# Optimization experiments

Measured on AMD Instinct MI355X. Metric: run time of the kernel, lower is better.

The kernel has to match this reference:

```python
import jax, jax.numpy as jnp
import numpy as np

N_NODES = 50000
N_EDGES = 800000
D_IN = 64
D_OUT = 64


def setup_inputs() -> dict:
    key = jax.random.key(0)
    k1, k2, k3, k4 = jax.random.split(key, 4)
    x = jax.random.normal(k1, (N_NODES, D_IN), dtype=jnp.float32)
    src = jax.random.randint(k2, (N_EDGES,), 0, N_NODES, dtype=jnp.int64)
    dst = jax.random.randint(k3, (N_EDGES,), 0, N_NODES, dtype=jnp.int64)
    W = jax.random.normal(k4, (D_IN, D_OUT), dtype=jnp.float32) / np.sqrt(D_IN)
    b = jnp.zeros((D_OUT,), dtype=jnp.float32)
    return {"x": x, "src": src, "dst": dst, "W": W, "b": b}


def reference(x, src, dst, W, b):
    # DGL GraphConv, norm='both': out = D_in^{-1/2} A D_out^{-1/2} x W + b
    n = x.shape[0]
    ones = jnp.ones(src.shape[0], dtype=x.dtype)
    out_deg = jax.ops.segment_sum(ones, src, num_segments=n)  # out-degree of each node
    in_deg = jax.ops.segment_sum(ones, dst, num_segments=n)   # in-degree of each node
    norm_src = jax.lax.rsqrt(jnp.clip(out_deg, 1.0))          # [N]
    norm_dst = jax.lax.rsqrt(jnp.clip(in_deg, 1.0))           # [N]
    h = x * norm_src[:, None]                                 # [N, D_in]
    msg = jnp.take(h, src, axis=0)                            # [E, D_in] gather
    agg = jax.ops.segment_sum(msg, dst, num_segments=n)       # [N, D_in] scatter-add
    agg = agg * norm_dst[:, None]
    return agg @ W + b                                        # [N, D_out]
```

## Files before the change

### kernel.cpp

```cpp
#include <hip/hip_runtime.h>
#include <hip/hip_fp16.h>

#define N_NODES 50000
#define N_EDGES 800000
#define D 64

#define SLICES 100
#define I4S    2000
#define NI4    200000
#define NWORDS 12512

typedef float vfloat2 __attribute__((ext_vector_type(2)));

#define CTR_OFF    0
#define BASE_OFF   256
#define END_OFF    200320
#define SNORM_OFF  400384
#define DNORM_OFF  600448
#define SSRC_OFF   800512
#define OCC_OFF    4000768
#define PART_OFF   4800768
#define YA_OFF     14810368
#define YB_OFF     18010624

__global__ __launch_bounds__(256) void degree_occ_kernel(const int4* __restrict__ src4,
                                                         const int4* __restrict__ dst4,
                                                         unsigned int* __restrict__ partial,
                                                         uchar4* __restrict__ occ4,
                                                         int* __restrict__ ctr) {
    __shared__ unsigned int hist[NWORDS];
    int tid = threadIdx.x;
    if (blockIdx.x == 0 && tid == 0) *ctr = 0;
    uint4* h4 = (uint4*)hist;
    for (int i = tid; i < NWORDS / 4; i += 256) h4[i] = make_uint4(0, 0, 0, 0);
    __syncthreads();

    int role  = blockIdx.x & 1;
    int slice = blockIdx.x >> 1;
    int beg = slice * I4S, end = beg + I4S;
    if (role == 0) {
        for (int i = beg + tid; i < end; i += 256) {
            int4 v = src4[i];
            atomicAdd(&hist[v.x >> 2], 1u << ((v.x & 3) * 8));
            atomicAdd(&hist[v.y >> 2], 1u << ((v.y & 3) * 8));
            atomicAdd(&hist[v.z >> 2], 1u << ((v.z & 3) * 8));
            atomicAdd(&hist[v.w >> 2], 1u << ((v.w & 3) * 8));
        }
    } else {
        for (int i = beg + tid; i < end; i += 256) {
            int4 v = dst4[i];
            unsigned int o0 = (atomicAdd(&hist[v.x >> 2], 1u << ((v.x & 3) * 8)) >> ((v.x & 3) * 8)) & 0xFFu;
            unsigned int o1 = (atomicAdd(&hist[v.y >> 2], 1u << ((v.y & 3) * 8)) >> ((v.y & 3) * 8)) & 0xFFu;
            unsigned int o2 = (atomicAdd(&hist[v.z >> 2], 1u << ((v.z & 3) * 8)) >> ((v.z & 3) * 8)) & 0xFFu;
            unsigned int o3 = (atomicAdd(&hist[v.w >> 2], 1u << ((v.w & 3) * 8)) >> ((v.w & 3) * 8)) & 0xFFu;
            occ4[i] = make_uchar4((unsigned char)o0, (unsigned char)o1,
                                  (unsigned char)o2, (unsigned char)o3);
        }
    }
    __syncthreads();

    uint4* p4 = (uint4*)(partial + (size_t)blockIdx.x * NWORDS);
    for (int i = tid; i < NWORDS / 4; i += 256) p4[i] = h4[i];
}

__global__ __launch_bounds__(256) void merge_scan_kernel(unsigned int* __restrict__ partial,
                                                         int* __restrict__ base,
                                                         int* __restrict__ rend,
                                                         float* __restrict__ snorm,
                                                         float* __restrict__ dnorm,
                                                         int* __restrict__ ctr) {
    int w = blockIdx.x * blockDim.x + threadIdx.x;
    int lane = threadIdx.x & 63;
    unsigned int accin = 0, accout = 0;
    if (w < 12500) {
        unsigned int* po = partial + w;
        unsigned int* pd = partial + NWORDS + w;
#pragma unroll 4
        for (int s = 0; s < SLICES; s++) {
            size_t off = (size_t)(2 * s) * NWORDS;
            accout += po[off];
            unsigned int v = pd[off];
            pd[off] = accin;
            accin += v;
        }
    }
    int d0 = accin & 0xFF, d1 = (accin >> 8) & 0xFF,
        d2 = (accin >> 16) & 0xFF, d3 = (accin >> 24) & 0xFF;
    int tsum = d0 + d1 + d2 + d3;
    int run = tsum;
#pragma unroll
    for (int off = 1; off < 64; off <<= 1) {
        int v = __shfl_up(run, off);
        if (lane >= off) run += v;
    }
    int wtot = __shfl(run, 63);
    int wbase = 0;
    if (lane == 63) wbase = atomicAdd(ctr, wtot);
    wbase = __shfl(wbase, 63);
    if (w < 12500) {
        int b0 = wbase + run - tsum;
        int b1 = b0 + d0, b2 = b1 + d1, b3 = b2 + d2;
        ((int4*)base)[w] = make_int4(b0, b1, b2, b3);
        ((int4*)rend)[w] = make_int4(b1, b2, b3, b3 + d3);
        ((float4*)dnorm)[w] = make_float4(rsqrtf(fmaxf((float)d0, 1.f)),
                                          rsqrtf(fmaxf((float)d1, 1.f)),
                                          rsqrtf(fmaxf((float)d2, 1.f)),
                                          rsqrtf(fmaxf((float)d3, 1.f)));
        int o0 = accout & 0xFF, o1 = (accout >> 8) & 0xFF,
            o2 = (accout >> 16) & 0xFF, o3 = (accout >> 24) & 0xFF;
        ((float4*)snorm)[w] = make_float4(rsqrtf(fmaxf((float)o0, 1.f)),
                                          rsqrtf(fmaxf((float)o1, 1.f)),
                                          rsqrtf(fmaxf((float)o2, 1.f)),
                                          rsqrtf(fmaxf((float)o3, 1.f)));
    }
}

#define FYBLK 1024
__global__ __launch_bounds__(256, 4) void filly_kernel(const int4* __restrict__ src4,
                                                       const int4* __restrict__ dst4,
                                                       const uchar4* __restrict__ occ4,
                                                       const unsigned int* __restrict__ partial,
                                                       const int* __restrict__ base,
                                                       int* __restrict__ ssrc,
                                                       const float* __restrict__ x,
                                                       const float* __restrict__ snorm,
                                                       const float* __restrict__ W,
                                                       __half* __restrict__ yA,
                                                       __half* __restrict__ yB) {
    int tid = blockIdx.x * blockDim.x + threadIdx.x;
    int lane = threadIdx.x & 63;

    if (tid < NI4) {
        int s = tid / I4S;
        const unsigned int* pref = partial + (size_t)(2 * s + 1) * NWORDS;
        int4 sv = src4[tid], tv = dst4[tid];
        uchar4 oc = occ4[tid];
#define FILL_ONE(T, S, O)                                                     \
        {                                                                     \
            int t = (T); int sh = (t & 3) * 8;                                \
            int p = base[t] + (int)((pref[t >> 2] >> sh) & 0xFFu) + (int)(O); \
            ssrc[p] = (S);                                                    \
        }
        FILL_ONE(tv.x, sv.x, oc.x)
        FILL_ONE(tv.y, sv.y, oc.y)
        FILL_ONE(tv.z, sv.z, oc.z)
        FILL_ONE(tv.w, sv.w, oc.w)
#undef FILL_ONE
    }

    float Wreg[D];
#pragma unroll
    for (int k = 0; k < D; k++) Wreg[k] = W[k * D + lane];
    __half* yh = (lane < 32) ? yA : yB;
    int jl = lane & 31;
    int wave = tid >> 6;
    const int nwaves = FYBLK * 4;
    for (int n = wave; n < N_NODES; n += nwaves) {
        float hv = x[(size_t)n * D + lane] * snorm[n];
        int hb = __float_as_int(hv);
        float p0 = 0.f, p1 = 0.f, p2 = 0.f, p3 = 0.f;
#pragma unroll
        for (int k = 0; k < D; k += 4) {
            p0 = fmaf(__int_as_float(__builtin_amdgcn_readlane(hb, k + 0)), Wreg[k + 0], p0);
            p1 = fmaf(__int_as_float(__builtin_amdgcn_readlane(hb, k + 1)), Wreg[k + 1], p1);
            p2 = fmaf(__int_as_float(__builtin_amdgcn_readlane(hb, k + 2)), Wreg[k + 2], p2);
            p3 = fmaf(__int_as_float(__builtin_amdgcn_readlane(hb, k + 3)), Wreg[k + 3], p3);
        }
        yh[(size_t)n * 32 + jl] = __float2half((p0 + p1) + (p2 + p3));
    }
}

#define GBLK 2048
__global__ __launch_bounds__(256, 8) void gather_kernel(const __half2* __restrict__ yA,
                                                        const __half2* __restrict__ yB,
                                                        const int* __restrict__ ssrc,
                                                        const int* __restrict__ base,
                                                        const int* __restrict__ rend,
                                                        const float* __restrict__ dnorm,
                                                        const float* __restrict__ bias,
                                                        float* __restrict__ out) {
    int lane = threadIdx.x & 63;
    int q = lane >> 4;
    int c = lane & 15;
    int pass = blockIdx.x & 1;
    int pblk = blockIdx.x >> 1;
    int wave = (pblk << 2) | (threadIdx.x >> 6);
    const int nwaves = (GBLK / 2) * 4;

    float2 b2 = ((const float2*)bias)[(pass << 4) + c];
    const __half2* ycol = (pass ? yB : yA) + c;

#define ACC(A, F) { (A).x += (F).x; (A).y += (F).y; }

    for (int n = wave; n < N_NODES; n += nwaves) {
        int beg = base[n], end = rend[n];
        float dn = dnorm[n];
        float2 a0 = make_float2(0.f, 0.f), a1 = a0, a2 = a0, a3 = a0;
        int i = beg;
        for (; i + 16 <= end; i += 16) {
            int s0 = ssrc[i + q],      s1 = ssrc[i + 4 + q];
            int s2 = ssrc[i + 8 + q],  s3 = ssrc[i + 12 + q];
            float2 f0 = __half22float2(ycol[(size_t)s0 * 16]);
            float2 f1 = __half22float2(ycol[(size_t)s1 * 16]);
            float2 f2 = __half22float2(ycol[(size_t)s2 * 16]);
            float2 f3 = __half22float2(ycol[(size_t)s3 * 16]);
            ACC(a0, f0) ACC(a1, f1) ACC(a2, f2) ACC(a3, f3)
        }
        for (; i + 4 <= end; i += 4) {
            int s = ssrc[i + q];
            float2 f = __half22float2(ycol[(size_t)s * 16]);
            ACC(a0, f)
        }
        int rem = end - i;
        if (q < rem) {
            int s = ssrc[i + q];
            float2 f = __half22float2(ycol[(size_t)s * 16]);
            ACC(a1, f)
        }
        float2 t;
        t.x = (a0.x + a1.x) + (a2.x + a3.x);
        t.y = (a0.y + a1.y) + (a2.y + a3.y);
        t.x += __shfl(t.x, lane ^ 16); t.y += __shfl(t.y, lane ^ 16);
        t.x += __shfl(t.x, lane ^ 32); t.y += __shfl(t.y, lane ^ 32);
        if (q == 0) {
            vfloat2 o;
            o.x = fmaf(t.x, dn, b2.x);
            o.y = fmaf(t.y, dn, b2.y);
            __builtin_nontemporal_store(o, (vfloat2*)(out + (size_t)n * D + (pass << 5)) + c);
        }
    }
#undef ACC
}

extern "C" void kernel_launch(void* const* d_in, const int* in_sizes, int n_in,
                              void* d_out, int out_size, void* d_ws, size_t ws_size,
                              hipStream_t stream) {
    const float* x   = (const float*)d_in[0];
    const int*   src = (const int*)d_in[1];
    const int*   dst = (const int*)d_in[2];
    const float* W   = (const float*)d_in[3];
    const float* b   = (const float*)d_in[4];
    float* out = (float*)d_out;

    char* ws = (char*)d_ws;
    int*          ctr   = (int*)(ws + CTR_OFF);
    int*          base  = (int*)(ws + BASE_OFF);
    int*          rend  = (int*)(ws + END_OFF);
    float*        snorm = (float*)(ws + SNORM_OFF);
    float*        dnorm = (float*)(ws + DNORM_OFF);
    int*          ssrc  = (int*)(ws + SSRC_OFF);
    uchar4*       occ4  = (uchar4*)(ws + OCC_OFF);
    unsigned int* part  = (unsigned int*)(ws + PART_OFF);
    __half*       yA    = (__half*)(ws + YA_OFF);
    __half*       yB    = (__half*)(ws + YB_OFF);

    const int4* src4 = (const int4*)src;
    const int4* dst4 = (const int4*)dst;

    degree_occ_kernel<<<2 * SLICES, 256, 0, stream>>>(src4, dst4, part, occ4, ctr);
    merge_scan_kernel<<<(12500 + 255) / 256, 256, 0, stream>>>(part, base, rend,
                                                               snorm, dnorm, ctr);
    filly_kernel<<<FYBLK, 256, 0, stream>>>(src4, dst4, occ4, part, base, ssrc,
                                            x, snorm, W, yA, yB);
    gather_kernel<<<GBLK, 256, 0, stream>>>((const __half2*)yA, (const __half2*)yB,
                                            ssrc, base, rend, dnorm, b, out);
}
```

Before: 149.4 us.

## Fuse merge-scan into fill kernel with a global gate and pack node metadata

Folds the merge/scan kernel into the fill/transform kernel. The first 49 blocks do the scan and signal a global atomic gate, and every block spins on it before filling the sorted source array. Base and degree are packed into one int2 meta array, and the gather computes the destination norm from the degree instead of loading a separate dnorm array. This removes one launch and its inter-kernel gap plus some memory traffic. In exchange it relies on all 1024 blocks being co-resident, or at least the merge blocks being scheduled, to avoid deadlock in the spin-wait.

```diff
diff --git a/kernel.cpp b/kernel.cpp
--- a/kernel.cpp
+++ b/kernel.cpp
@@ -9,28 +9,30 @@
 #define I4S    2000
 #define NI4    200000
 #define NWORDS 12512
+#define MBLK   1024
+#define MERGE_BLOCKS 49
 
 typedef float vfloat2 __attribute__((ext_vector_type(2)));
 
 #define CTR_OFF    0
-#define BASE_OFF   256
-#define END_OFF    200320
+#define GATE_OFF   64
+#define META_OFF   256
 #define SNORM_OFF  400384
-#define DNORM_OFF  600448
-#define SSRC_OFF   800512
-#define OCC_OFF    4000768
-#define PART_OFF   4800768
-#define YA_OFF     14810368
-#define YB_OFF     18010624
+#define SSRC_OFF   600576
+#define OCC_OFF    3800576
+#define PART_OFF   4600832
+#define YA_OFF     14610432
+#define YB_OFF     17810688
 
 __global__ __launch_bounds__(256) void degree_occ_kernel(const int4* __restrict__ src4,
                                                          const int4* __restrict__ dst4,
                                                          unsigned int* __restrict__ partial,
                                                          uchar4* __restrict__ occ4,
-                                                         int* __restrict__ ctr) {
+                                                         int* __restrict__ ctr,
+                                                         int* __restrict__ gate) {
     __shared__ unsigned int hist[NWORDS];
     int tid = threadIdx.x;
-    if (blockIdx.x == 0 && tid == 0) *ctr = 0;
+    if (blockIdx.x == 0 && tid == 0) { *ctr = 0; *gate = 0; }
     uint4* h4 = (uint4*)hist;
     for (int i = tid; i < NWORDS / 4; i += 256) h4[i] = make_uint4(0, 0, 0, 0);
     __syncthreads();
@@ -63,82 +65,85 @@
     for (int i = tid; i < NWORDS / 4; i += 256) p4[i] = h4[i];
 }
 
-__global__ __launch_bounds__(256) void merge_scan_kernel(unsigned int* __restrict__ partial,
-                                                         int* __restrict__ base,
-                                                         int* __restrict__ rend,
-                                                         float* __restrict__ snorm,
-                                                         float* __restrict__ dnorm,
-                                                         int* __restrict__ ctr) {
-    int w = blockIdx.x * blockDim.x + threadIdx.x;
-    int lane = threadIdx.x & 63;
-    unsigned int accin = 0, accout = 0;
-    if (w < 12500) {
-        unsigned int* po = partial + w;
-        unsigned int* pd = partial + NWORDS + w;
-#pragma unroll 4
-        for (int s = 0; s < SLICES; s++) {
-            size_t off = (size_t)(2 * s) * NWORDS;
-            accout += po[off];
-            unsigned int v = pd[off];
-            pd[off] = accin;
-            accin += v;
-        }
-    }
-    int d0 = accin & 0xFF, d1 = (accin >> 8) & 0xFF,
-        d2 = (accin >> 16) & 0xFF, d3 = (accin >> 24) & 0xFF;
-    int tsum = d0 + d1 + d2 + d3;
-    int run = tsum;
-#pragma unroll
-    for (int off = 1; off < 64; off <<= 1) {
-        int v = __shfl_up(run, off);
-        if (lane >= off) run += v;
-    }
-    int wtot = __shfl(run, 63);
-    int wbase = 0;
-    if (lane == 63) wbase = atomicAdd(ctr, wtot);
-    wbase = __shfl(wbase, 63);
-    if (w < 12500) {
-        int b0 = wbase + run - tsum;
-        int b1 = b0 + d0, b2 = b1 + d1, b3 = b2 + d2;
-        ((int4*)base)[w] = make_int4(b0, b1, b2, b3);
-        ((int4*)rend)[w] = make_int4(b1, b2, b3, b3 + d3);
-        ((float4*)dnorm)[w] = make_float4(rsqrtf(fmaxf((float)d0, 1.f)),
-                                          rsqrtf(fmaxf((float)d1, 1.f)),
-                                          rsqrtf(fmaxf((float)d2, 1.f)),
-                                          rsqrtf(fmaxf((float)d3, 1.f)));
-        int o0 = accout & 0xFF, o1 = (accout >> 8) & 0xFF,
-            o2 = (accout >> 16) & 0xFF, o3 = (accout >> 24) & 0xFF;
-        ((float4*)snorm)[w] = make_float4(rsqrtf(fmaxf((float)o0, 1.f)),
-                                          rsqrtf(fmaxf((float)o1, 1.f)),
-                                          rsqrtf(fmaxf((float)o2, 1.f)),
-                                          rsqrtf(fmaxf((float)o3, 1.f)));
-    }
-}
-
-#define FYBLK 1024
-__global__ __launch_bounds__(256, 4) void filly_kernel(const int4* __restrict__ src4,
-                                                       const int4* __restrict__ dst4,
-                                                       const uchar4* __restrict__ occ4,
-                                                       const unsigned int* __restrict__ partial,
-                                                       const int* __restrict__ base,
-                                                       int* __restrict__ ssrc,
-                                                       const float* __restrict__ x,
-                                                       const float* __restrict__ snorm,
-                                                       const float* __restrict__ W,
-                                                       __half* __restrict__ yA,
-                                                       __half* __restrict__ yB) {
+__global__ __launch_bounds__(256, 4) void mega_kernel(const int4* __restrict__ src4,
+                                                      const int4* __restrict__ dst4,
+                                                      const uchar4* __restrict__ occ4,
+                                                      unsigned int* __restrict__ partial,
+                                                      int2* __restrict__ meta,
+                                                      float* __restrict__ snorm,
+                                                      int* __restrict__ ctr,
+                                                      int* __restrict__ gate,
+                                                      int* __restrict__ ssrc,
+                                                      const float* __restrict__ x,
+                                                      const float* __restrict__ W,
+                                                      __half* __restrict__ yA,
+                                                      __half* __restrict__ yB) {
     int tid = blockIdx.x * blockDim.x + threadIdx.x;
     int lane = threadIdx.x & 63;
 
-    if (tid < NI4) {
+    int4 sv, tv; uchar4 oc;
+    bool havefill = (tid < NI4);
+    if (havefill) { sv = src4[tid]; tv = dst4[tid]; oc = occ4[tid]; }
+
+    if (blockIdx.x < MERGE_BLOCKS) {
+        int w = tid;
+        unsigned int accin = 0, accout = 0;
+        bool act = (w < 12500);
+        if (act) {
+            unsigned int* po = partial + w;
+            unsigned int* pd = partial + NWORDS + w;
+#pragma unroll 4
+            for (int s = 0; s < SLICES; s++) {
+                size_t off = (size_t)(2 * s) * NWORDS;
+                accout += po[off];
+                unsigned int v = pd[off];
+                pd[off] = accin;
+                accin += v;
+            }
+        }
+        int d0 = accin & 0xFF, d1 = (accin >> 8) & 0xFF,
+            d2 = (accin >> 16) & 0xFF, d3 = (accin >> 24) & 0xFF;
+        int tsum = d0 + d1 + d2 + d3;
+        int run = tsum;
+#pragma unroll
+        for (int off = 1; off < 64; off <<= 1) {
+            int v = __shfl_up(run, off);
+            if (lane >= off) run += v;
+        }
+        int wtot = __shfl(run, 63);
+        int wbase = 0;
+        if (lane == 63) wbase = atomicAdd(ctr, wtot);
+        wbase = __shfl(wbase, 63);
+        if (act) {
+            int b0 = wbase + run - tsum;
+            int b1 = b0 + d0, b2 = b1 + d1, b3 = b2 + d2;
+            ((int4*)meta)[2 * w]     = make_int4(b0, d0, b1, d1);
+            ((int4*)meta)[2 * w + 1] = make_int4(b2, d2, b3, d3);
+            int o0 = accout & 0xFF, o1 = (accout >> 8) & 0xFF,
+                o2 = (accout >> 16) & 0xFF, o3 = (accout >> 24) & 0xFF;
+            ((float4*)snorm)[w] = make_float4(rsqrtf(fmaxf((float)o0, 1.f)),
+                                              rsqrtf(fmaxf((float)o1, 1.f)),
+                                              rsqrtf(fmaxf((float)o2, 1.f)),
+                                              rsqrtf(fmaxf((float)o3, 1.f)));
+        }
+        __threadfence();
+        __syncthreads();
+        if (threadIdx.x == 0) atomicAdd(gate, 1);
+    }
+
+    if (threadIdx.x == 0) {
+        while (atomicAdd(gate, 0) < MERGE_BLOCKS) __builtin_amdgcn_s_sleep(8);
+    }
+    __syncthreads();
+    __threadfence();
+
+    if (havefill) {
         int s = tid / I4S;
         const unsigned int* pref = partial + (size_t)(2 * s + 1) * NWORDS;
-        int4 sv = src4[tid], tv = dst4[tid];
-        uchar4 oc = occ4[tid];
 #define FILL_ONE(T, S, O)                                                     \
         {                                                                     \
             int t = (T); int sh = (t & 3) * 8;                                \
-            int p = base[t] + (int)((pref[t >> 2] >> sh) & 0xFFu) + (int)(O); \
+            int p = meta[t].x + (int)((pref[t >> 2] >> sh) & 0xFFu) + (int)(O); \
             ssrc[p] = (S);                                                    \
         }
         FILL_ONE(tv.x, sv.x, oc.x)
@@ -154,7 +159,7 @@
     __half* yh = (lane < 32) ? yA : yB;
     int jl = lane & 31;
     int wave = tid >> 6;
-    const int nwaves = FYBLK * 4;
+    const int nwaves = MBLK * 4;
     for (int n = wave; n < N_NODES; n += nwaves) {
         float hv = x[(size_t)n * D + lane] * snorm[n];
         int hb = __float_as_int(hv);
@@ -174,9 +179,7 @@
 __global__ __launch_bounds__(256, 8) void gather_kernel(const __half2* __restrict__ yA,
                                                         const __half2* __restrict__ yB,
                                                         const int* __restrict__ ssrc,
-                                                        const int* __restrict__ base,
-                                                        const int* __restrict__ rend,
-                                                        const float* __restrict__ dnorm,
+                                                        const int2* __restrict__ meta,
                                                         const float* __restrict__ bias,
                                                         float* __restrict__ out) {
     int lane = threadIdx.x & 63;
@@ -193,8 +196,9 @@
 #define ACC(A, F) { (A).x += (F).x; (A).y += (F).y; }
 
     for (int n = wave; n < N_NODES; n += nwaves) {
-        int beg = base[n], end = rend[n];
-        float dn = dnorm[n];
+        int2 m = meta[n];
+        int beg = m.x, end = m.x + m.y;
+        float dn = rsqrtf(fmaxf((float)m.y, 1.0f));
         float2 a0 = make_float2(0.f, 0.f), a1 = a0, a2 = a0, a3 = a0;
         int i = beg;
         for (; i + 16 <= end; i += 16) {
@@ -244,10 +248,9 @@
 
     char* ws = (char*)d_ws;
     int*          ctr   = (int*)(ws + CTR_OFF);
-    int*          base  = (int*)(ws + BASE_OFF);
-    int*          rend  = (int*)(ws + END_OFF);
+    int*          gate  = (int*)(ws + GATE_OFF);
+    int2*         meta  = (int2*)(ws + META_OFF);
     float*        snorm = (float*)(ws + SNORM_OFF);
-    float*        dnorm = (float*)(ws + DNORM_OFF);
     int*          ssrc  = (int*)(ws + SSRC_OFF);
     uchar4*       occ4  = (uchar4*)(ws + OCC_OFF);
     unsigned int* part  = (unsigned int*)(ws + PART_OFF);
@@ -257,11 +260,9 @@
     const int4* src4 = (const int4*)src;
     const int4* dst4 = (const int4*)dst;
 
-    degree_occ_kernel<<<2 * SLICES, 256, 0, stream>>>(src4, dst4, part, occ4, ctr);
-    merge_scan_kernel<<<(12500 + 255) / 256, 256, 0, stream>>>(part, base, rend,
-                                                               snorm, dnorm, ctr);
-    filly_kernel<<<FYBLK, 256, 0, stream>>>(src4, dst4, occ4, part, base, ssrc,
-                                            x, snorm, W, yA, yB);
+    degree_occ_kernel<<<2 * SLICES, 256, 0, stream>>>(src4, dst4, part, occ4, ctr, gate);
+    mega_kernel<<<MBLK, 256, 0, stream>>>(src4, dst4, occ4, part, meta, snorm,
+                                          ctr, gate, ssrc, x, W, yA, yB);
     gather_kernel<<<GBLK, 256, 0, stream>>>((const __half2*)yA, (const __half2*)yB,
-                                            ssrc, base, rend, dnorm, b, out);
-}
+                                            ssrc, meta, b, out);
+}
```

Result: slower. 230.2 us (+54.1%).
